# Performance work log

Hardware: AMD Instinct MI355X
Metric: run time of the kernel (lower is better)

## Reference

```python
import jax, jax.numpy as jnp
import numpy as np

P = 16          # patch size
GH = GW = 29    # grid (464/16)
N = GH * GW     # 841 tokens
E = 384         # embed dim
NH = 6          # heads
HD = E // NH    # 64
DEPTH = 8
EPS = 1e-5


def _dist_bias():
    g = jnp.linspace(0.0, 1.0, GH)
    gy, gx = jnp.meshgrid(g, g, indexing='ij')
    coords = jnp.stack([gy.ravel(), gx.ravel()], axis=-1)        # [N,2]
    d2 = ((coords[None, :, :] - coords[:, None, :]) ** 2).sum(-1)  # [N,N]
    return -d2 / d2.max()                                        # in [-1,0]


def _ln(x, g, b):
    m = x.mean(-1, keepdims=True)
    v = ((x - m) ** 2).mean(-1, keepdims=True)
    return (x - m) * jax.lax.rsqrt(v + EPS) * g + b


def _shift(x, dy, dx):
    # zero-pad shift, matching F.pad default 'constant' mode in the source
    B, C, H, W = x.shape
    if dy > 0:
        x = jnp.pad(x, ((0, 0), (0, 0), (dy, 0), (0, 0)))[:, :, :H, :]
    elif dy < 0:
        x = jnp.pad(x, ((0, 0), (0, 0), (0, -dy), (0, 0)))[:, :, -H:, :]
    if dx > 0:
        x = jnp.pad(x, ((0, 0), (0, 0), (0, 0), (dx, 0)))[:, :, :, :W]
    elif dx < 0:
        x = jnp.pad(x, ((0, 0), (0, 0), (0, 0), (0, -dx)))[:, :, :, -W:]
    return x


def _patchify(x):
    B, C, H, W = x.shape
    gh, gw = H // P, W // P
    x = x.reshape(B, C, gh, P, gw, P)
    x = x.transpose(0, 2, 4, 1, 3, 5)         # [B,gh,gw,C,p,p]
    return x.reshape(B, gh * gw, C * P * P)


def setup_inputs() -> dict:
    key = jax.random.key(0)
    ks = jax.random.split(key, 8)
    D = DEPTH
    s = 0.02
    inp = {
        'x': jax.random.normal(ks[0], (16, 3, 464, 464), jnp.float32),
        'tok_ng': jnp.ones((3840,), jnp.float32),
        'tok_nb': jnp.zeros((3840,), jnp.float32),
        'tok_w1': jax.random.normal(ks[1], (3840, 768), jnp.float32) * s,
        'tok_b1': jnp.zeros((768,), jnp.float32),
        'tok_w2': jax.random.normal(ks[2], (768, 384), jnp.float32) * s,
        'tok_b2': jnp.zeros((384,), jnp.float32),
        'ln1_g': jnp.ones((D, E), jnp.float32),
        'ln1_b': jnp.zeros((D, E), jnp.float32),
        'w_qkv': jax.random.normal(ks[3], (D, E, 3 * E), jnp.float32) * s,
        'temp': jnp.full((D, NH), np.log(HD ** -0.5), jnp.float32),
        'loc_w': jnp.full((D, NH), 0.1, jnp.float32),
        'w_proj': jax.random.normal(ks[4], (D, E, E), jnp.float32) * s,
        'b_proj': jnp.zeros((D, E), jnp.float32),
        'ls1': jnp.full((D, E), 1e-4, jnp.float32),
        'ln2_g': jnp.ones((D, E), jnp.float32),
        'ln2_b': jnp.zeros((D, E), jnp.float32),
        'ff_w1': jax.random.normal(ks[5], (D, E, 4 * E), jnp.float32) * s,
        'ff_b1': jnp.zeros((D, 4 * E), jnp.float32),
        'ff_w2': jax.random.normal(ks[6], (D, 4 * E, E), jnp.float32) * s,
        'ff_b2': jnp.zeros((D, E), jnp.float32),
        'ls2': jnp.full((D, E), 1e-4, jnp.float32),
    }
    return inp


def _forward(x, tok_ng, tok_nb, tok_w1, tok_b1, tok_w2, tok_b2,
             ln1_g, ln1_b, w_qkv, temp, loc_w, w_proj, b_proj, ls1,
             ln2_g, ln2_b, ff_w1, ff_b1, ff_w2, ff_b2, ls2):
    p2 = P // 2
    shifts = [x, _shift(x, p2, 0), _shift(x, -p2, 0), _shift(x, 0, p2), _shift(x, 0, -p2)]
    patches = jnp.concatenate([_patchify(s) for s in shifts], axis=-1)  # [B,N,3840]
    h = _ln(patches, tok_ng, tok_nb)
    h = jax.nn.gelu(h @ tok_w1 + tok_b1, approximate=False)
    h = h @ tok_w2 + tok_b2                                             # [B,N,E]

    loc = _dist_bias()                                                  # [N,N]

    def block(h, p):
        (g1, b1, wqkv, tp, lw, wp, bp, l1, g2, b2, fw1, fb1, fw2, fb2, l2) = p
        y = _ln(h, g1, b1)
        qkv = (y @ wqkv).reshape(h.shape[0], N, 3, NH, HD)
        qkv = qkv.transpose(2, 0, 3, 1, 4)                              # [3,B,H,N,hd]
        q, k, v = qkv[0], qkv[1], qkv[2]
        scale = jnp.exp(tp)[:, None, None]                              # per-head temperature
        logits = jnp.einsum('bhnd,bhmd->bhnm', q, k) * scale
        logits = logits + lw[:, None, None] * loc                       # per-head locality bias
        a = jax.nn.softmax(logits, axis=-1)
        o = jnp.einsum('bhnm,bhmd->bhnd', a, v)
        o = o.transpose(0, 2, 1, 3).reshape(h.shape[0], N, E)
        h = h + l1 * (o @ wp + bp)
        y2 = _ln(h, g2, b2)
        f = jax.nn.gelu(y2 @ fw1 + fb1, approximate=False) @ fw2 + fb2
        h = h + l2 * f
        return h, None

    params = (ln1_g, ln1_b, w_qkv, temp, loc_w, w_proj, b_proj, ls1,
              ln2_g, ln2_b, ff_w1, ff_b1, ff_w2, ff_b2, ls2)
    h, _ = jax.lax.scan(block, h, params)
    return h


def reference(x, tok_ng, tok_nb, tok_w1, tok_b1, tok_w2, tok_b2,
              ln1_g, ln1_b, w_qkv, temp, loc_w, w_proj, b_proj, ls1,
              ln2_g, ln2_b, ff_w1, ff_b1, ff_w2, ff_b2, ls2):
    return _forward(x, tok_ng, tok_nb, tok_w1, tok_b1, tok_w2, tok_b2,
                    ln1_g, ln1_b, w_qkv, temp, loc_w, w_proj, b_proj, ls1,
                    ln2_g, ln2_b, ff_w1, ff_b1, ff_w2, ff_b2, ls2)
```

## Files before the change

kernel.cpp:

```cpp
#include <hip/hip_runtime.h>
#include <math.h>

typedef __attribute__((ext_vector_type(8))) short short8;
typedef __attribute__((ext_vector_type(4))) float f32x4;
typedef unsigned short u16;

#define NTOK 841
#define GRID_H 29
#define E_ 384
#define NH_ 6
#define MROWS 13456
#define MP 13568
#define MQ 14336
#define CM 5120

__device__ __forceinline__ u16 f2bf(float f) {
  union { float f; unsigned int u; } c; c.f = f;
  unsigned int u = c.u;
  return (u16)((u + 0x7fffu + ((u >> 16) & 1u)) >> 16);
}

__device__ __forceinline__ float bf2f(u16 b) {
  union { unsigned int u; float f; } c; c.u = ((unsigned int)b) << 16; return c.f;
}

__device__ __forceinline__ float gelu_exact(float v) {
  return 0.5f * v * (1.f + erff(v * 0.70710678118654752440f));
}

__device__ __forceinline__ float fexp2(float x) {
  float r; asm("v_exp_f32 %0, %1" : "=v"(r) : "v"(x)); return r;
}

__device__ __forceinline__ int swz64(int row, int col) {
  return row * 128 + ((((col >> 3) ^ (row & 7)) << 4) | ((col & 7) << 1));
}

__global__ __launch_bounds__(256) void transpose_conv(const float* __restrict__ in,
    u16* __restrict__ out, int K, int N) {
  __shared__ float tile[32][33];
  size_t zo = (size_t)blockIdx.z * K * N;
  const float* inp = in + zo;
  u16* outp = out + zo;
  int n0 = blockIdx.x * 32, k0 = blockIdx.y * 32;
  int tx = threadIdx.x & 31, ty = threadIdx.x >> 5;
  #pragma unroll
  for (int r = ty; r < 32; r += 8) tile[r][tx] = inp[(size_t)(k0 + r) * N + n0 + tx];
  __syncthreads();
  #pragma unroll
  for (int r = ty; r < 32; r += 8) outp[(size_t)(n0 + r) * K + k0 + tx] = f2bf(tile[tx][r]);
}

__global__ __launch_bounds__(256) void patch_ln(const float* __restrict__ x,
    const float* __restrict__ g, const float* __restrict__ bsh, u16* __restrict__ out,
    int t0) {
  int t = t0 + blockIdx.x;
  int tid = threadIdx.x;
  u16* orow = out + (size_t)blockIdx.x * 3840;
  if (t >= MROWS) {
    #pragma unroll
    for (int j = 0; j < 15; ++j) orow[tid + j * 256] = 0;
    return;
  }
  int bimg = t / NTOK, n = t % NTOK;
  int gy = n / GRID_H, gx = n % GRID_H;
  float vals[15];
  float s1 = 0.f, s2 = 0.f;
  #pragma unroll
  for (int j = 0; j < 15; ++j) {
    int cout = tid + j * 256;
    int s = cout / 768, rem = cout % 768;
    int c = rem / 256, rem2 = rem % 256;
    int py = rem2 / 16, px = rem2 % 16;
    int dy = (s == 1 ? 8 : 0) - (s == 2 ? 8 : 0);
    int dx = (s == 3 ? 8 : 0) - (s == 4 ? 8 : 0);
    int Y = gy * 16 + py - dy;
    int X = gx * 16 + px - dx;
    float v = 0.f;
    if (Y >= 0 && Y < 464 && X >= 0 && X < 464)
      v = x[(((size_t)bimg * 3 + c) * 464 + Y) * 464 + X];
    vals[j] = v;
    s1 += v; s2 += v * v;
  }
  #pragma unroll
  for (int m = 1; m < 64; m <<= 1) { s1 += __shfl_xor(s1, m); s2 += __shfl_xor(s2, m); }
  __shared__ float ws1[4], ws2[4];
  int wid = tid >> 6;
  if ((tid & 63) == 0) { ws1[wid] = s1; ws2[wid] = s2; }
  __syncthreads();
  s1 = ws1[0] + ws1[1] + ws1[2] + ws1[3];
  s2 = ws2[0] + ws2[1] + ws2[2] + ws2[3];
  float mean = s1 * (1.f / 3840.f);
  float var = s2 * (1.f / 3840.f) - mean * mean;
  float rs = rsqrtf(var + 1e-5f);
  #pragma unroll
  for (int j = 0; j < 15; ++j) {
    int cout = tid + j * 256;
    orow[cout] = f2bf((vals[j] - mean) * rs * g[cout] + bsh[cout]);
  }
}

__global__ __launch_bounds__(256) void ln384(const float* __restrict__ h,
    const float* __restrict__ g, const float* __restrict__ bsh, u16* __restrict__ y) {
  int row = blockIdx.x * 4 + (threadIdx.x >> 6);
  int lane = threadIdx.x & 63;
  const float* hr = h + (size_t)row * E_;
  float v[6];
  float s1 = 0.f;
  #pragma unroll
  for (int j = 0; j < 6; ++j) { v[j] = hr[lane + j * 64]; s1 += v[j]; }
  #pragma unroll
  for (int m = 1; m < 64; m <<= 1) s1 += __shfl_xor(s1, m);
  float mean = s1 * (1.f / 384.f);
  float s2 = 0.f;
  #pragma unroll
  for (int j = 0; j < 6; ++j) { float d = v[j] - mean; s2 += d * d; }
  #pragma unroll
  for (int m = 1; m < 64; m <<= 1) s2 += __shfl_xor(s2, m);
  float rs = rsqrtf(s2 * (1.f / 384.f) + 1e-5f);
  u16* yr = y + (size_t)row * E_;
  #pragma unroll
  for (int j = 0; j < 6; ++j) {
    int c = lane + j * 64;
    yr[c] = f2bf((v[j] - mean) * rs * g[c] + bsh[c]);
  }
}

__global__ __launch_bounds__(256) void ln384p(const float* __restrict__ h,
    const float* __restrict__ g, const float* __restrict__ bsh, u16* __restrict__ yp) {
  int rowp = blockIdx.x * 4 + (threadIdx.x >> 6);
  int lane = threadIdx.x & 63;
  int bg = rowp / 896, tk = rowp - bg * 896;
  u16* yr = yp + (size_t)rowp * E_;
  if (tk >= NTOK) {
    #pragma unroll
    for (int j = 0; j < 6; ++j) yr[lane + j * 64] = 0;
    return;
  }
  const float* hr = h + (size_t)(bg * NTOK + tk) * E_;
  float v[6];
  float s1 = 0.f;
  #pragma unroll
  for (int j = 0; j < 6; ++j) { v[j] = hr[lane + j * 64]; s1 += v[j]; }
  #pragma unroll
  for (int m = 1; m < 64; m <<= 1) s1 += __shfl_xor(s1, m);
  float mean = s1 * (1.f / 384.f);
  float s2 = 0.f;
  #pragma unroll
  for (int j = 0; j < 6; ++j) { float d = v[j] - mean; s2 += d * d; }
  #pragma unroll
  for (int m = 1; m < 64; m <<= 1) s2 += __shfl_xor(s2, m);
  float rs = rsqrtf(s2 * (1.f / 384.f) + 1e-5f);
  #pragma unroll
  for (int j = 0; j < 6; ++j) {
    int c = lane + j * 64;
    yr[c] = f2bf((v[j] - mean) * rs * g[c] + bsh[c]);
  }
}

template<int EPI, int TM>
__global__ __launch_bounds__(256) void gemm_bt(
    const u16* __restrict__ A, const u16* __restrict__ BT,
    int N, int K,
    const float* __restrict__ bias, const float* __restrict__ lscale,
    float* __restrict__ resid, u16* __restrict__ outb, float* __restrict__ outf) {
  constexpr int MI = TM / 32;
  constexpr int BUF = (TM + 128) * 64;
  __shared__ alignas(16) char smem[2 * BUF * 2];
  short* As = (short*)smem;
  const int gx = gridDim.x;
  const int nwg = gx * gridDim.y;
  int L = blockIdx.x + blockIdx.y * gx;
  int q8 = nwg >> 3, r8 = nwg & 7, xcd = L & 7, pos = L >> 3;
  int L2 = (xcd < r8 ? xcd * (q8 + 1) : r8 * (q8 + 1) + (xcd - r8) * q8) + pos;
  const int m0 = (L2 / gx) * TM, n0 = (L2 % gx) * 128;
  const int tid = threadIdx.x;
  const int lane = tid & 63, wid = tid >> 6;
  const int wm = wid >> 1, wn = wid & 1;
  const int rowl = lane >> 3;
  const int colc = (((lane & 7) ^ (rowl & 7)) << 3);
  f32x4 acc[MI][4] = {};
  const int nkt = K >> 6;

  auto stage = [&](int b, int kt) {
    short* Ab = As + b * BUF;
    short* Bb = Ab + TM * 64;
    const int k0 = kt * 64;
    #pragma unroll
    for (int i = 0; i < TM / 32; ++i) {
      int chunk = i * 4 + wid;
      const u16* ga = A + (size_t)(m0 + chunk * 8 + rowl) * K + k0 + colc;
      __builtin_amdgcn_global_load_lds((const __attribute__((address_space(1))) void*)ga,
          (__attribute__((address_space(3))) void*)(Ab + (chunk << 9)), 16, 0, 0);
    }
    #pragma unroll
    for (int i = 0; i < 4; ++i) {
      int chunk = i * 4 + wid;
      const u16* gb = BT + (size_t)(n0 + chunk * 8 + rowl) * K + k0 + colc;
      __builtin_amdgcn_global_load_lds((const __attribute__((address_space(1))) void*)gb,
          (__attribute__((address_space(3))) void*)(Bb + (chunk << 9)), 16, 0, 0);
    }
  };

  stage(0, 0);
  for (int kt = 0; kt < nkt; ++kt) {
    const int cur = kt & 1;
    if (kt + 1 < nkt) {
      stage(cur ^ 1, kt + 1);
      if (TM == 128) asm volatile("s_waitcnt vmcnt(8)" ::: "memory");
      else           asm volatile("s_waitcnt vmcnt(6)" ::: "memory");
    } else {
      asm volatile("s_waitcnt vmcnt(0)" ::: "memory");
    }
    __builtin_amdgcn_s_barrier();
    __builtin_amdgcn_sched_barrier(0);
    short* Ab = As + cur * BUF;
    short* Bb = Ab + TM * 64;
    #pragma unroll
    for (int kk = 0; kk < 2; ++kk) {
      short8 a[MI], bfr[4];
      #pragma unroll
      for (int mi = 0; mi < MI; ++mi) {
        int ra = wm * (TM / 2) + mi * 16 + (lane & 15);
        a[mi] = *(const short8*)(Ab + ra * 64 + ((((kk << 2) | (lane >> 4)) ^ (ra & 7)) << 3));
      }
      #pragma unroll
      for (int nj = 0; nj < 4; ++nj) {
        int rb = wn * 64 + nj * 16 + (lane & 15);
        bfr[nj] = *(const short8*)(Bb + rb * 64 + ((((kk << 2) | (lane >> 4)) ^ (rb & 7)) << 3));
      }
      #pragma unroll
      for (int mi = 0; mi < MI; ++mi)
        #pragma unroll
        for (int nj = 0; nj < 4; ++nj)
          acc[mi][nj] = __builtin_amdgcn_mfma_f32_16x16x32_bf16(a[mi], bfr[nj], acc[mi][nj], 0, 0, 0);
    }
    __builtin_amdgcn_s_barrier();
  }
  const int rrow = (lane >> 4) << 2;
  const int ccol = lane & 15;
  if (EPI == 1) {
    u16* Cs = (u16*)smem;
    __syncthreads();
    #pragma unroll
    for (int mi = 0; mi < MI; ++mi)
      #pragma unroll
      for (int nj = 0; nj < 4; ++nj) {
        int cc = wn * 64 + nj * 16 + ccol;
        float bi = bias[n0 + cc];
        #pragma unroll
        for (int r = 0; r < 4; ++r) {
          int cr = wm * (TM / 2) + mi * 16 + rrow + r;
          Cs[cr * 136 + cc] = f2bf(gelu_exact(acc[mi][nj][r] + bi));
        }
      }
    __syncthreads();
    #pragma unroll
    for (int it = 0; it < TM / 16; ++it) {
      int idx = it * 256 + tid;
      int orow = idx >> 4, c = idx & 15;
      short8 v = *(const short8*)(Cs + orow * 136 + c * 8);
      *(short8*)(outb + (size_t)(m0 + orow) * N + n0 + c * 8) = v;
    }
    return;
  }
  #pragma unroll
  for (int mi = 0; mi < MI; ++mi)
    #pragma unroll
    for (int nj = 0; nj < 4; ++nj) {
      int gn = n0 + wn * 64 + nj * 16 + ccol;
      #pragma unroll
      for (int r = 0; r < 4; ++r) {
        int gm = m0 + wm * (TM / 2) + mi * 16 + rrow + r;
        float v = acc[mi][nj][r];
        if (EPI == 2) {
          outf[(size_t)gm * N + gn] = v + bias[gn];
        } else {
          float* p = resid + (size_t)gm * N + gn;
          *p = *p + lscale[gn] * (v + bias[gn]);
        }
      }
    }
}

__global__ __launch_bounds__(256) void gemm_qkv(
    const u16* __restrict__ A, const u16* __restrict__ BT,
    u16* __restrict__ Qp, u16* __restrict__ Kp, u16* __restrict__ Vp) {
  const int K = 384;
  constexpr int BUF = 256 * 64;
  __shared__ alignas(16) char smem[2 * BUF * 2];
  short* As = (short*)smem;
  int L = blockIdx.x + blockIdx.y * 9;
  int L2 = (L & 7) * 126 + (L >> 3);
  const int m0 = (L2 / 9) * 128, n0 = (L2 % 9) * 128;
  const int tid = threadIdx.x;
  const int lane = tid & 63, wid = tid >> 6;
  const int wm = wid >> 1, wn = wid & 1;
  const int rowl = lane >> 3;
  const int colc = (((lane & 7) ^ (rowl & 7)) << 3);
  f32x4 acc[4][4] = {};

  auto stage = [&](int b, int kt) {
    short* Ab = As + b * BUF;
    short* Bb = Ab + 128 * 64;
    const int k0 = kt * 64;
    #pragma unroll
    for (int i = 0; i < 4; ++i) {
      int chunk = i * 4 + wid;
      const u16* ga = A + (size_t)(m0 + chunk * 8 + rowl) * K + k0 + colc;
      __builtin_amdgcn_global_load_lds((const __attribute__((address_space(1))) void*)ga,
          (__attribute__((address_space(3))) void*)(Ab + (chunk << 9)), 16, 0, 0);
      const u16* gb = BT + (size_t)(n0 + chunk * 8 + rowl) * K + k0 + colc;
      __builtin_amdgcn_global_load_lds((const __attribute__((address_space(1))) void*)gb,
          (__attribute__((address_space(3))) void*)(Bb + (chunk << 9)), 16, 0, 0);
    }
  };

  stage(0, 0);
  for (int kt = 0; kt < 6; ++kt) {
    const int cur = kt & 1;
    if (kt + 1 < 6) {
      stage(cur ^ 1, kt + 1);
      asm volatile("s_waitcnt vmcnt(8)" ::: "memory");
    } else {
      asm volatile("s_waitcnt vmcnt(0)" ::: "memory");
    }
    __builtin_amdgcn_s_barrier();
    __builtin_amdgcn_sched_barrier(0);
    short* Ab = As + cur * BUF;
    short* Bb = Ab + 128 * 64;
    #pragma unroll
    for (int kk = 0; kk < 2; ++kk) {
      short8 a[4], bfr[4];
      #pragma unroll
      for (int mi = 0; mi < 4; ++mi) {
        int ra = wm * 64 + mi * 16 + (lane & 15);
        a[mi] = *(const short8*)(Ab + ra * 64 + ((((kk << 2) | (lane >> 4)) ^ (ra & 7)) << 3));
      }
      #pragma unroll
      for (int nj = 0; nj < 4; ++nj) {
        int rb = wn * 64 + nj * 16 + (lane & 15);
        bfr[nj] = *(const short8*)(Bb + rb * 64 + ((((kk << 2) | (lane >> 4)) ^ (rb & 7)) << 3));
      }
      #pragma unroll
      for (int mi = 0; mi < 4; ++mi)
        #pragma unroll
        for (int nj = 0; nj < 4; ++nj)
          acc[mi][nj] = __builtin_amdgcn_mfma_f32_16x16x32_bf16(a[mi], bfr[nj], acc[mi][nj], 0, 0, 0);
    }
    __builtin_amdgcn_s_barrier();
  }
  const int seg = n0 / 384;
  const int h0 = (n0 - seg * 384) >> 6;
  const int bg = m0 / 896;
  const int tk0 = m0 - bg * 896;
  const int rrow = (lane >> 4) << 2;
  const int ccol = lane & 15;
  u16* Cs = (u16*)smem;
  __syncthreads();
  #pragma unroll
  for (int mi = 0; mi < 4; ++mi)
    #pragma unroll
    for (int nj = 0; nj < 4; ++nj) {
      int cc = wn * 64 + nj * 16 + ccol;
      #pragma unroll
      for (int r = 0; r < 4; ++r) {
        int cr = wm * 64 + mi * 16 + rrow + r;
        u16 bv = f2bf(acc[mi][nj][r]);
        if (seg == 2) Cs[cc * 136 + cr] = bv;
        else          Cs[cr * 136 + cc] = bv;
      }
    }
  __syncthreads();
  #pragma unroll
  for (int i = 0; i < 8; ++i) {
    int idx = i * 256 + tid;
    int c = idx & 7;
    int orow = idx >> 3;
    int hs = orow >> 7;
    int rl = orow & 127;
    size_t bh = (size_t)(bg * 6 + h0 + hs);
    if (seg == 2) {
      int tile_l = rl >> 6, hd = rl & 63;
      short8 v = *(const short8*)(Cs + (hs * 64 + hd) * 136 + tile_l * 64 + c * 8);
      int tile = (tk0 >> 6) + tile_l;
      *(short8*)(Vp + bh * 57344 + tile * 4096 + hd * 64 + ((c ^ (hd & 7)) << 3)) = v;
    } else {
      short8 v = *(const short8*)(Cs + rl * 136 + hs * 64 + c * 8);
      if (seg == 0) {
        *(short8*)(Qp + (bh * 896 + tk0 + rl) * 64 + c * 8) = v;
      } else {
        int tok = tk0 + rl;
        *(short8*)(Kp + bh * 57344 + (tok >> 6) * 4096 + (tok & 63) * 64 + ((c ^ (tok & 7)) << 3)) = v;
      }
    }
  }
}

__global__ __launch_bounds__(256) void attn_sk(const u16* __restrict__ Qp,
    const u16* __restrict__ Kp, const u16* __restrict__ Vp,
    const float* __restrict__ temp_d, const float* __restrict__ locw_d,
    u16* __restrict__ op, float* __restrict__ ml) {
  int Lw = blockIdx.x + 14 * blockIdx.z + 28 * blockIdx.y;
  int L2 = (Lw & 7) * 336 + (Lw >> 3);
  const int bh = L2 / 28;
  const int rem = L2 % 28;
  const int ks = rem / 14, qt = rem % 14;
  const int hh = bh % NH_;
  const int tid = threadIdx.x, lane = tid & 63, w = tid >> 6;
  const int lg = lane >> 4, lc = lane & 15;
  const float LOG2E = 1.44269504088896f;
  const float scale = __expf(temp_d[hh]) * LOG2E;
  const float lwh = locw_d[hh] * LOG2E * -0.5f;
  const int kb0 = ks * 448;

  __shared__ alignas(16) char ktl[64 * 128];
  __shared__ alignas(16) char vtl[64 * 128];
  __shared__ alignas(16) char pl[4][16 * 128];
  __shared__ float yx2[896 * 2];

  for (int j = tid; j < 896; j += 256) {
    unsigned jc = j < NTOK ? (unsigned)j : (NTOK - 1);
    yx2[j * 2]     = (float)(jc / 29u) * (1.f / 28.f);
    yx2[j * 2 + 1] = (float)(jc % 29u) * (1.f / 28.f);
  }

  const char* qb = (const char*)(Qp + ((size_t)bh * 896 + qt * 64) * 64);
  short8 qf0 = *(const short8*)(qb + (w * 16 + lc) * 128 + lg * 16);
  short8 qf1 = *(const short8*)(qb + (w * 16 + lc) * 128 + 64 + lg * 16);

  const char* kbase = (const char*)Kp + ((size_t)bh * 14 + ks * 7) * 8192;
  const char* vbase = (const char*)Vp + ((size_t)bh * 14 + ks * 7) * 8192;

  auto stage = [&](int kt) {
    #pragma unroll
    for (int i = 0; i < 2; ++i) {
      int off = (i * 4 + w) * 1024;
      __builtin_amdgcn_global_load_lds(
          (const __attribute__((address_space(1))) void*)(kbase + kt * 8192 + off + lane * 16),
          (__attribute__((address_space(3))) void*)(ktl + off), 16, 0, 0);
      __builtin_amdgcn_global_load_lds(
          (const __attribute__((address_space(1))) void*)(vbase + kt * 8192 + off + lane * 16),
          (__attribute__((address_space(3))) void*)(vtl + off), 16, 0, 0);
    }
  };

  f32x4 of[4] = {};
  float mrow[4], psum[4];
  #pragma unroll
  for (int r = 0; r < 4; ++r) { mrow[r] = -3e38f; psum[r] = 0.f; }

  stage(0);
  __syncthreads();

  float qy[4], qx[4];
  #pragma unroll
  for (int r = 0; r < 4; ++r) {
    int iq = qt * 64 + w * 16 + (lg << 2) + r;
    qy[r] = yx2[iq * 2];
    qx[r] = yx2[iq * 2 + 1];
  }

  for (int kt = 0; kt < 7; ++kt) {
    f32x4 sf[4];
    __builtin_amdgcn_s_setprio(1);
    #pragma unroll
    for (int nt = 0; nt < 4; ++nt) {
      short8 kf0 = *(const short8*)(ktl + swz64(nt * 16 + lc, lg << 3));
      short8 kf1 = *(const short8*)(ktl + swz64(nt * 16 + lc, 32 + (lg << 3)));
      f32x4 z = {0.f, 0.f, 0.f, 0.f};
      z = __builtin_amdgcn_mfma_f32_16x16x32_bf16(qf0, kf0, z, 0, 0, 0);
      z = __builtin_amdgcn_mfma_f32_16x16x32_bf16(qf1, kf1, z, 0, 0, 0);
      sf[nt] = z;
    }
    __builtin_amdgcn_s_setprio(0);

    #pragma unroll
    for (int nt = 0; nt < 4; ++nt) {
      int j = kb0 + kt * 64 + nt * 16 + lc;
      float jy = yx2[j * 2], jx = yx2[j * 2 + 1];
      #pragma unroll
      for (int r = 0; r < 4; ++r) {
        float dy = qy[r] - jy, dx = qx[r] - jx;
        float val = sf[nt][r] * scale + lwh * (dy * dy + dx * dx);
        sf[nt][r] = (j < NTOK) ? val : -3e38f;
      }
    }

    float lm[4];
    #pragma unroll
    for (int r = 0; r < 4; ++r)
      lm[r] = fmaxf(fmaxf(sf[0][r], sf[1][r]), fmaxf(sf[2][r], sf[3][r]));
    bool trig = (lm[0] > mrow[0] + 12.f) | (lm[1] > mrow[1] + 12.f) |
                (lm[2] > mrow[2] + 12.f) | (lm[3] > mrow[3] + 12.f);
    if (__any(trig)) {
      #pragma unroll
      for (int r = 0; r < 4; ++r) {
        float tm = lm[r];
        #pragma unroll
        for (int m = 1; m < 16; m <<= 1) tm = fmaxf(tm, __shfl_xor(tm, m));
        float mnew = fmaxf(mrow[r], tm);
        float alpha = fexp2(mrow[r] - mnew);
        psum[r] *= alpha;
        of[0][r] *= alpha; of[1][r] *= alpha; of[2][r] *= alpha; of[3][r] *= alpha;
        mrow[r] = mnew;
      }
    }

    char* plw = pl[w];
    #pragma unroll
    for (int nt = 0; nt < 4; ++nt)
      #pragma unroll
      for (int r = 0; r < 4; ++r) {
        float p = fexp2(sf[nt][r] - mrow[r]);
        psum[r] += p;
        *(u16*)(plw + swz64((lg << 2) + r, nt * 16 + lc)) = f2bf(p);
      }
    asm volatile("s_waitcnt lgkmcnt(0)" ::: "memory");
    __builtin_amdgcn_sched_barrier(0);
    short8 pa[2];
    #pragma unroll
    for (int t = 0; t < 2; ++t)
      pa[t] = *(const short8*)(plw + swz64(lc, t * 32 + (lg << 3)));

    __builtin_amdgcn_s_setprio(1);
    #pragma unroll
    for (int n2 = 0; n2 < 4; ++n2) {
      f32x4 accv = of[n2];
      #pragma unroll
      for (int t = 0; t < 2; ++t) {
        short8 vf = *(const short8*)(vtl + swz64(n2 * 16 + lc, t * 32 + (lg << 3)));
        accv = __builtin_amdgcn_mfma_f32_16x16x32_bf16(pa[t], vf, accv, 0, 0, 0);
      }
      of[n2] = accv;
    }
    __builtin_amdgcn_s_setprio(0);

    if (kt < 6) {
      __syncthreads();
      stage(kt + 1);
      __syncthreads();
    }
  }

  #pragma unroll
  for (int r = 0; r < 4; ++r) {
    float s = psum[r];
    #pragma unroll
    for (int m = 1; m < 16; m <<= 1) s += __shfl_xor(s, m);
    int iq = qt * 64 + w * 16 + (lg << 2) + r;
    if (iq < NTOK) {
      size_t rb = (size_t)(ks * 96 + bh) * 896 + iq;
      #pragma unroll
      for (int n2 = 0; n2 < 4; ++n2)
        op[rb * 64 + n2 * 16 + lc] = f2bf(of[n2][r]);
      if (lc == 0) { ml[rb * 2] = mrow[r]; ml[rb * 2 + 1] = s; }
    }
  }
}

__global__ __launch_bounds__(256) void combine(const u16* __restrict__ op,
    const float* __restrict__ ml, u16* __restrict__ ob) {
  const int bh = blockIdx.y, bimg = bh / NH_, hh = bh % NH_;
  const int wid = threadIdx.x >> 6, lane = threadIdx.x & 63;
  const int tokb = blockIdx.x * 16 + wid * 4;
  #pragma unroll
  for (int rr = 0; rr < 4; ++rr) {
    int tok = tokb + rr;
    if (tok >= NTOK) return;
    size_t i1 = (size_t)bh * 896 + tok;
    size_t i2 = (size_t)(96 + bh) * 896 + tok;
    float m1 = ml[i1 * 2], l1 = ml[i1 * 2 + 1];
    float m2 = ml[i2 * 2], l2 = ml[i2 * 2 + 1];
    float m = fmaxf(m1, m2);
    float w1 = fexp2(m1 - m), w2 = fexp2(m2 - m);
    float inv = 1.f / (l1 * w1 + l2 * w2);
    float o1 = bf2f(op[i1 * 64 + lane]);
    float o2 = bf2f(op[i2 * 64 + lane]);
    ob[((size_t)(bimg * NTOK + tok)) * E_ + hh * 64 + lane] =
        f2bf((o1 * w1 + o2 * w2) * inv);
  }
}

__global__ __launch_bounds__(256) void copy_out(const float* __restrict__ h, float* __restrict__ out) {
  size_t i = (size_t)blockIdx.x * 256 + threadIdx.x;
  if (i < (size_t)MROWS * E_) out[i] = h[i];
}

extern "C" void kernel_launch(void* const* d_in, const int* in_sizes, int n_in,
                              void* d_out, int out_size, void* d_ws, size_t ws_size,
                              hipStream_t stream) {
  const float* x      = (const float*)d_in[0];
  const float* tok_ng = (const float*)d_in[1];
  const float* tok_nb = (const float*)d_in[2];
  const float* tok_w1 = (const float*)d_in[3];
  const float* tok_b1 = (const float*)d_in[4];
  const float* tok_w2 = (const float*)d_in[5];
  const float* tok_b2 = (const float*)d_in[6];
  const float* ln1_g  = (const float*)d_in[7];
  const float* ln1_b  = (const float*)d_in[8];
  const float* w_qkv  = (const float*)d_in[9];
  const float* temp   = (const float*)d_in[10];
  const float* loc_w  = (const float*)d_in[11];
  const float* w_proj = (const float*)d_in[12];
  const float* b_proj = (const float*)d_in[13];
  const float* ls1    = (const float*)d_in[14];
  const float* ln2_g  = (const float*)d_in[15];
  const float* ln2_b  = (const float*)d_in[16];
  const float* ff_w1  = (const float*)d_in[17];
  const float* ff_b1  = (const float*)d_in[18];
  const float* ff_w2  = (const float*)d_in[19];
  const float* ff_b2  = (const float*)d_in[20];
  const float* ls2    = (const float*)d_in[21];
  float* out = (float*)d_out;

  char* ws = (char*)d_ws;
  size_t off = 0;
  auto alloc = [&](size_t bytes) -> void* {
    void* p = ws + off; off += (bytes + 255) & ~(size_t)255; return p;
  };
  u16* w1T   = (u16*)alloc(768UL * 3840 * 2);
  u16* w2T   = (u16*)alloc(384UL * 768 * 2);
  u16* qkvT  = (u16*)alloc(8UL * 1152 * 384 * 2);
  u16* projT = (u16*)alloc(8UL * 384 * 384 * 2);
  u16* f1T   = (u16*)alloc(8UL * 1536 * 384 * 2);
  u16* f2T   = (u16*)alloc(8UL * 384 * 1536 * 2);
  float* h   = (float*)alloc((size_t)MP * 384 * 4);
  char* regB = (char*)alloc(22500000);
  u16* h1   = (u16*)regB;
  u16* ypad = (u16*)regB;
  u16* yff  = (u16*)regB;
  u16* ob   = (u16*)(regB + 11010048);
  char* regA = (char*)alloc((size_t)MP * 1536 * 2);
  u16* Xlnc = (u16*)regA;
  u16* Qp   = (u16*)regA;
  u16* Kp   = (u16*)(regA + 11010048);
  u16* Vp   = (u16*)(regA + 22020096);
  u16* f1b  = (u16*)regA;
  u16* op   = (u16*)alloc(2UL * 96 * 896 * 64 * 2);
  float* ml = (float*)alloc(2UL * 96 * 896 * 2 * 4);
  (void)in_sizes; (void)n_in; (void)out_size;

  if (off > ws_size) return;

  transpose_conv<<<dim3(24, 120, 1), 256, 0, stream>>>(tok_w1, w1T, 3840, 768);
  transpose_conv<<<dim3(12, 24, 1), 256, 0, stream>>>(tok_w2, w2T, 768, 384);
  transpose_conv<<<dim3(36, 12, 8), 256, 0, stream>>>(w_qkv, qkvT, 384, 1152);
  transpose_conv<<<dim3(12, 12, 8), 256, 0, stream>>>(w_proj, projT, 384, 384);
  transpose_conv<<<dim3(48, 12, 8), 256, 0, stream>>>(ff_w1, f1T, 384, 1536);
  transpose_conv<<<dim3(12, 48, 8), 256, 0, stream>>>(ff_w2, f2T, 1536, 384);

  for (int m = 0; m < MP; m += CM) {
    int rows = MP - m; if (rows > CM) rows = CM;
    patch_ln<<<rows, 256, 0, stream>>>(x, tok_ng, tok_nb, Xlnc, m);
    gemm_bt<1, 128><<<dim3(6, rows / 128), 256, 0, stream>>>(Xlnc, w1T, 768, 3840,
        tok_b1, nullptr, nullptr, h1 + (size_t)m * 768, nullptr);
  }
  gemm_bt<2, 64><<<dim3(3, MP / 64), 256, 0, stream>>>(h1, w2T, 384, 768, tok_b2,
      nullptr, nullptr, nullptr, h);

  for (int d = 0; d < 8; ++d) {
    ln384p<<<MQ / 4, 256, 0, stream>>>(h, ln1_g + d * E_, ln1_b + d * E_, ypad);
    gemm_qkv<<<dim3(9, 112), 256, 0, stream>>>(ypad, qkvT + (size_t)d * 1152 * 384, Qp, Kp, Vp);
    attn_sk<<<dim3(14, 96, 2), 256, 0, stream>>>(Qp, Kp, Vp, temp + d * NH_, loc_w + d * NH_, op, ml);
    combine<<<dim3(53, 96), 256, 0, stream>>>(op, ml, ob);
    gemm_bt<3, 64><<<dim3(3, MP / 64), 256, 0, stream>>>(ob, projT + (size_t)d * 384 * 384,
        384, 384, b_proj + d * E_, ls1 + d * E_, h, nullptr, nullptr);
    ln384<<<MP / 4, 256, 0, stream>>>(h, ln2_g + d * E_, ln2_b + d * E_, yff);
    gemm_bt<1, 128><<<dim3(12, MP / 128), 256, 0, stream>>>(yff, f1T + (size_t)d * 1536 * 384,
        1536, 384, ff_b1 + d * 1536, nullptr, nullptr, f1b, nullptr);
    gemm_bt<3, 64><<<dim3(3, MP / 64), 256, 0, stream>>>(f1b, f2T + (size_t)d * 384 * 1536,
        384, 1536, ff_b2 + d * E_, ls2 + d * E_, h, nullptr, nullptr);
  }

  copy_out<<<(MROWS * E_ + 255) / 256, 256, 0, stream>>>(h, out);
}
```

Baseline: 1.912 ms.

## Double-buffer K/V tiles in attention kernel and prefetch next tile

Attention kernel now keeps two LDS buffers for K and V and issues the global-to-LDS load for the next tile before computing on the current one. This replaces the two full barriers per iteration with one waitcnt plus barrier. It also moves the out-of-range key masking into a branch taken only on the last partial tile, and flattens the launch grid to 1D. LDS use per block grows, which may lower occupancy.

```diff
diff --git a/kernel.cpp b/kernel.cpp
--- a/kernel.cpp
+++ b/kernel.cpp
@@ -401,7 +401,7 @@
     const u16* __restrict__ Kp, const u16* __restrict__ Vp,
     const float* __restrict__ temp_d, const float* __restrict__ locw_d,
     u16* __restrict__ op, float* __restrict__ ml) {
-  int Lw = blockIdx.x + 14 * blockIdx.z + 28 * blockIdx.y;
+  int Lw = blockIdx.x;
   int L2 = (Lw & 7) * 336 + (Lw >> 3);
   const int bh = L2 / 28;
   const int rem = L2 % 28;
@@ -414,9 +414,9 @@
   const float lwh = locw_d[hh] * LOG2E * -0.5f;
   const int kb0 = ks * 448;
 
-  __shared__ alignas(16) char ktl[64 * 128];
-  __shared__ alignas(16) char vtl[64 * 128];
-  __shared__ alignas(16) char pl[4][16 * 128];
+  __shared__ alignas(16) char ktl[2][8192];
+  __shared__ alignas(16) char vtl[2][8192];
+  __shared__ alignas(16) char pl[4][2048];
   __shared__ float yx2[896 * 2];
 
   for (int j = tid; j < 896; j += 256) {
@@ -432,16 +432,16 @@
   const char* kbase = (const char*)Kp + ((size_t)bh * 14 + ks * 7) * 8192;
   const char* vbase = (const char*)Vp + ((size_t)bh * 14 + ks * 7) * 8192;
 
-  auto stage = [&](int kt) {
+  auto stage = [&](int b, int kt) {
     #pragma unroll
     for (int i = 0; i < 2; ++i) {
       int off = (i * 4 + w) * 1024;
       __builtin_amdgcn_global_load_lds(
           (const __attribute__((address_space(1))) void*)(kbase + kt * 8192 + off + lane * 16),
-          (__attribute__((address_space(3))) void*)(ktl + off), 16, 0, 0);
+          (__attribute__((address_space(3))) void*)(ktl[b] + off), 16, 0, 0);
       __builtin_amdgcn_global_load_lds(
           (const __attribute__((address_space(1))) void*)(vbase + kt * 8192 + off + lane * 16),
-          (__attribute__((address_space(3))) void*)(vtl + off), 16, 0, 0);
+          (__attribute__((address_space(3))) void*)(vtl[b] + off), 16, 0, 0);
     }
   };
 
@@ -450,7 +450,8 @@
   #pragma unroll
   for (int r = 0; r < 4; ++r) { mrow[r] = -3e38f; psum[r] = 0.f; }
 
-  stage(0);
+  stage(0, 0);
+  asm volatile("s_waitcnt vmcnt(0)" ::: "memory");
   __syncthreads();
 
   float qy[4], qx[4];
@@ -462,12 +463,17 @@
   }
 
   for (int kt = 0; kt < 7; ++kt) {
+    const int b = kt & 1;
+    if (kt < 6) stage(b ^ 1, kt + 1);
+
+    const char* kb = ktl[b];
+    const char* vb = vtl[b];
     f32x4 sf[4];
     __builtin_amdgcn_s_setprio(1);
     #pragma unroll
     for (int nt = 0; nt < 4; ++nt) {
-      short8 kf0 = *(const short8*)(ktl + swz64(nt * 16 + lc, lg << 3));
-      short8 kf1 = *(const short8*)(ktl + swz64(nt * 16 + lc, 32 + (lg << 3)));
+      short8 kf0 = *(const short8*)(kb + swz64(nt * 16 + lc, lg << 3));
+      short8 kf1 = *(const short8*)(kb + swz64(nt * 16 + lc, 32 + (lg << 3)));
       f32x4 z = {0.f, 0.f, 0.f, 0.f};
       z = __builtin_amdgcn_mfma_f32_16x16x32_bf16(qf0, kf0, z, 0, 0, 0);
       z = __builtin_amdgcn_mfma_f32_16x16x32_bf16(qf1, kf1, z, 0, 0, 0);
@@ -475,15 +481,23 @@
     }
     __builtin_amdgcn_s_setprio(0);
 
+    const int jb = kb0 + kt * 64;
     #pragma unroll
     for (int nt = 0; nt < 4; ++nt) {
-      int j = kb0 + kt * 64 + nt * 16 + lc;
+      int j = jb + nt * 16 + lc;
       float jy = yx2[j * 2], jx = yx2[j * 2 + 1];
       #pragma unroll
       for (int r = 0; r < 4; ++r) {
         float dy = qy[r] - jy, dx = qx[r] - jx;
-        float val = sf[nt][r] * scale + lwh * (dy * dy + dx * dx);
-        sf[nt][r] = (j < NTOK) ? val : -3e38f;
+        sf[nt][r] = sf[nt][r] * scale + lwh * (dy * dy + dx * dx);
+      }
+    }
+    if (jb + 64 > NTOK) {
+      #pragma unroll
+      for (int nt = 0; nt < 4; ++nt) {
+        if (jb + nt * 16 + lc >= NTOK) {
+          sf[nt][0] = -3e38f; sf[nt][1] = -3e38f; sf[nt][2] = -3e38f; sf[nt][3] = -3e38f;
+        }
       }
     }
 
@@ -529,7 +543,7 @@
       f32x4 accv = of[n2];
       #pragma unroll
       for (int t = 0; t < 2; ++t) {
-        short8 vf = *(const short8*)(vtl + swz64(n2 * 16 + lc, t * 32 + (lg << 3)));
+        short8 vf = *(const short8*)(vb + swz64(n2 * 16 + lc, t * 32 + (lg << 3)));
         accv = __builtin_amdgcn_mfma_f32_16x16x32_bf16(pa[t], vf, accv, 0, 0, 0);
       }
       of[n2] = accv;
@@ -537,9 +551,9 @@
     __builtin_amdgcn_s_setprio(0);
 
     if (kt < 6) {
-      __syncthreads();
-      stage(kt + 1);
-      __syncthreads();
+      asm volatile("s_waitcnt vmcnt(0) lgkmcnt(0)" ::: "memory");
+      __builtin_amdgcn_sched_barrier(0);
+      __builtin_amdgcn_s_barrier();
     }
   }
 
@@ -662,7 +676,7 @@
   for (int d = 0; d < 8; ++d) {
     ln384p<<<MQ / 4, 256, 0, stream>>>(h, ln1_g + d * E_, ln1_b + d * E_, ypad);
     gemm_qkv<<<dim3(9, 112), 256, 0, stream>>>(ypad, qkvT + (size_t)d * 1152 * 384, Qp, Kp, Vp);
-    attn_sk<<<dim3(14, 96, 2), 256, 0, stream>>>(Qp, Kp, Vp, temp + d * NH_, loc_w + d * NH_, op, ml);
+    attn_sk<<<2688, 256, 0, stream>>>(Qp, Kp, Vp, temp + d * NH_, loc_w + d * NH_, op, ml);
     combine<<<dim3(53, 96), 256, 0, stream>>>(op, ml, ob);
     gemm_bt<3, 64><<<dim3(3, MP / 64), 256, 0, stream>>>(ob, projT + (size_t)d * 384 * 384,
         384, 384, b_proj + d * E_, ls1 + d * E_, h, nullptr, nullptr);
```

Result: no change. 1.897 ms (-0.8%).
